# Kernel tuning notes

Hardware: AMD Instinct MI355X
Metric: run time of the kernel (lower is better)

Reference implementation:

```python
import jax, jax.numpy as jnp
import numpy as np

IMG_SIZE = 416
STRIDES = (8, 16, 32)
NUM_CLASSES = 43
RADIUS = 1
ALPHA, GAMMA = 0.25, 2.0
LAMBDA_CLS, LAMBDA_BOX, LAMBDA_OBJ = 0.5, 7.5, 1.0


def _bce_logits(x, t):
    # stable binary_cross_entropy_with_logits, elementwise
    return jnp.maximum(x, 0.0) - x * t + jnp.log1p(jnp.exp(-jnp.abs(x)))


def _focal(x, t):
    bce = _bce_logits(x, t)
    pt = jnp.exp(-bce)
    return ALPHA * (1.0 - pt) ** GAMMA * bce


def _decode_boxes(reg_flat, stride, H, W):
    # reg_flat: [B, H*W, 4] -> boxes [B, H*W, 4] in pixel x1y1x2y2
    gy, gx = jnp.meshgrid(jnp.arange(H), jnp.arange(W), indexing='ij')
    grid = jnp.stack([gx, gy], axis=-1).reshape(-1, 2).astype(reg_flat.dtype)  # [A,2]
    xy = (grid[None] + reg_flat[..., :2]) * stride
    wh = jnp.exp(jnp.clip(reg_flat[..., 2:], -10.0, 10.0)) * stride
    return jnp.concatenate([xy - wh * 0.5, xy + wh * 0.5], axis=-1)


def _iou(pb, tb):
    # elementwise IoU over last dim=4 boxes; pb, tb: [..., 4]
    ix1 = jnp.maximum(pb[..., 0], tb[..., 0])
    iy1 = jnp.maximum(pb[..., 1], tb[..., 1])
    ix2 = jnp.minimum(pb[..., 2], tb[..., 2])
    iy2 = jnp.minimum(pb[..., 3], tb[..., 3])
    inter = jnp.clip(ix2 - ix1, 0.0) * jnp.clip(iy2 - iy1, 0.0)
    pa = (pb[..., 2] - pb[..., 0]) * (pb[..., 3] - pb[..., 1])
    ta = (tb[..., 2] - tb[..., 0]) * (tb[..., 3] - tb[..., 1])
    return inter / (pa + ta - inter + 1e-7)


def _assign(bboxes_px, labels, stride, H, W, C):
    # Vectorized SimpleCenterAssigner. Sequential scan over max_obj preserves
    B, M = labels.shape
    A = H * W
    cx = (bboxes_px[..., 0] + bboxes_px[..., 2]) * 0.5  # [B,M]
    cy = (bboxes_px[..., 1] + bboxes_px[..., 3]) * 0.5
    gx = jnp.clip((cx / stride).astype(jnp.int32), 0, W - 1)
    gy = jnp.clip((cy / stride).astype(jnp.int32), 0, H - 1)
    valid = labels >= 0
    offs = jnp.arange(-RADIUS, RADIUS + 1)
    dys, dxs = jnp.meshgrid(offs, offs, indexing='ij')
    dys, dxs = dys.reshape(-1), dxs.reshape(-1)  # [K=9]
    K = dys.shape[0]
    b_idx = jnp.broadcast_to(jnp.arange(B)[:, None], (B, K))

    def step(carry, xs):
        tl, tb, ts, fg = carry
        gx_m, gy_m, lab_m, box_m, val_m = xs  # one gt per batch element
        ax = gx_m[:, None] + dxs[None, :]  # [B,K]
        ay = gy_m[:, None] + dys[None, :]
        inb = (ax >= 0) & (ax < W) & (ay >= 0) & (ay < H) & val_m[:, None]
        idx = jnp.where(inb, ay * W + ax, A)  # invalid writes routed to pad slot A
        lab_c = jnp.clip(lab_m, 0, C - 1)
        fg = fg.at[b_idx, idx].set(True)
        tl = tl.at[b_idx, idx].set(jnp.broadcast_to(lab_m[:, None], (B, K)))
        tb = tb.at[b_idx, idx].set(jnp.broadcast_to(box_m[:, None, :], (B, K, 4)))
        ts = ts.at[b_idx, idx, jnp.broadcast_to(lab_c[:, None], (B, K))].set(1.0)
        return (tl, tb, ts, fg), None

    init = (jnp.full((B, A + 1), -1, jnp.int32),
            jnp.zeros((B, A + 1, 4), bboxes_px.dtype),
            jnp.zeros((B, A + 1, C), bboxes_px.dtype),
            jnp.zeros((B, A + 1), bool))
    xs = (gx.T, gy.T, labels.T, jnp.transpose(bboxes_px, (1, 0, 2)), valid.T)
    (tl, tb, ts, fg), _ = jax.lax.scan(step, init, xs)
    return tl[:, :A], tb[:, :A], ts[:, :A], fg[:, :A]


def _scale_loss(cls, reg, obj, bboxes_px, labels, stride, C):
    B, _, H, W = cls.shape
    A = H * W
    cls_f = jnp.transpose(cls, (0, 2, 3, 1)).reshape(B, A, C)
    reg_f = jnp.transpose(reg, (0, 2, 3, 1)).reshape(B, A, 4)
    obj_f = jnp.transpose(obj, (0, 2, 3, 1)).reshape(B, A)
    boxes = _decode_boxes(reg_f, stride, H, W)
    _, tb, ts, fg = _assign(bboxes_px, labels, stride, H, W, C)
    fgf = fg.astype(cls_f.dtype)
    num_fg = jnp.maximum(fgf.sum(), 1.0)
    # focal loss mean over [num_fg, C] selected elements
    cls_loss = (_focal(cls_f, ts) * fgf[..., None]).sum() / (num_fg * C)
    # IoU loss mean over fg anchors
    box_loss = ((1.0 - _iou(boxes, tb)) * fgf).sum() / num_fg
    # obj BCE sum over all anchors / num_fg, target = fg mask
    obj_loss = _bce_logits(obj_f, fgf).sum() / num_fg
    return cls_loss, box_loss, obj_loss


def _v3_loss(cls0, reg0, obj0, cls1, reg1, obj1, cls2, reg2, obj2, bboxes, labels):
    bboxes_px = bboxes * IMG_SIZE
    preds = [(cls0, reg0, obj0), (cls1, reg1, obj1), (cls2, reg2, obj2)]
    tot_cls = tot_box = tot_obj = 0.0
    for (c, r, o), s in zip(preds, STRIDES):
        cl, bl, ol = _scale_loss(c, r, o, bboxes_px, labels, s, NUM_CLASSES)
        tot_cls = tot_cls + cl
        tot_box = tot_box + bl
        tot_obj = tot_obj + ol
    n = len(preds)
    return (LAMBDA_CLS * tot_cls + LAMBDA_BOX * tot_box + LAMBDA_OBJ * tot_obj) / n


def setup_inputs() -> dict:
    key = jax.random.key(0)
    ks = jax.random.split(key, 12)
    B, M = 128, 50
    shapes = [(52, 43), (52, 4), (52, 1), (26, 43), (26, 4), (26, 1), (13, 43), (13, 4), (13, 1)]
    names = ['cls0', 'reg0', 'obj0', 'cls1', 'reg1', 'obj1', 'cls2', 'reg2', 'obj2']
    inp = {}
    for i, (nm, (hw, c)) in enumerate(zip(names, shapes)):
        inp[nm] = jax.random.normal(ks[i], (B, c, hw, hw), dtype=jnp.float32)
    # normalized [0,1] x1y1x2y2 gt boxes with x1<x2, y1<y2
    u = jax.random.uniform(ks[9], (B, M, 4), dtype=jnp.float32)
    cx, cy = u[..., 0], u[..., 1]
    w = 0.02 + 0.2 * u[..., 2]
    h = 0.02 + 0.2 * u[..., 3]
    inp['bboxes'] = jnp.stack([jnp.clip(cx - w / 2, 0, 1), jnp.clip(cy - h / 2, 0, 1),
                               jnp.clip(cx + w / 2, 0, 1), jnp.clip(cy + h / 2, 0, 1)], axis=-1)
    inp['labels'] = jax.random.randint(ks[10], (B, M), 0, 43, dtype=jnp.int32)
    return inp


def reference(cls0, reg0, obj0, cls1, reg1, obj1, cls2, reg2, obj2, bboxes, labels):
    return _v3_loss(cls0, reg0, obj0, cls1, reg1, obj1, cls2, reg2, obj2, bboxes, labels)
```

## Files before the change

### kernel.cpp

```cpp
#include <hip/hip_runtime.h>
#include <math.h>

#define BB 128
#define MM 50
#define CC 43
#define IMGF 416.0f

#define NBLK0 1408
#define NBLK01 1792
#define NBLK_TOTAL 1920

__device__ __forceinline__ float focal_fast(float x, bool t) {
    float e = __expf(-fabsf(x));
    float denom = 1.0f + e;
    float l = __logf(denom);
    float bce = fmaxf(x, 0.0f) - (t ? x : 0.0f) + l;
    float r = __builtin_amdgcn_rcpf(denom);
    float sig = (x >= 0.0f) ? r : e * r;
    float pt = t ? sig : 1.0f - sig;
    float om = 1.0f - pt;
    return 0.25f * om * om * bce;
}

__device__ __forceinline__ float bce_fast(float x, bool t) {
    float e = __expf(-fabsf(x));
    float l = __logf(1.0f + e);
    return fmaxf(x, 0.0f) - (t ? x : 0.0f) + l;
}

__global__ __launch_bounds__(256) void v3_main(
    const float* __restrict__ cls0, const float* __restrict__ reg0, const float* __restrict__ obj0,
    const float* __restrict__ cls1, const float* __restrict__ reg1, const float* __restrict__ obj1,
    const float* __restrict__ cls2, const float* __restrict__ reg2, const float* __restrict__ obj2,
    const float* __restrict__ bboxes, const int* __restrict__ labels,
    float* __restrict__ partials)
{
    const int bid = blockIdx.x;
    int s, b, chunk;
    if (bid < NBLK0)       { s = 0; b = bid / 11; chunk = bid - 11 * b; }
    else if (bid < NBLK01) { int r = bid - NBLK0; s = 1; b = r / 3; chunk = r - 3 * b; }
    else                   { s = 2; b = bid - NBLK01; chunk = 0; }

    int W, A; float strd, inv_strd;
    const float *cls, *reg, *obj;
    if (s == 0)      { W = 52; A = 2704; strd = 8.f;  inv_strd = 0.125f;   cls = cls0; reg = reg0; obj = obj0; }
    else if (s == 1) { W = 26; A = 676;  strd = 16.f; inv_strd = 0.0625f;  cls = cls1; reg = reg1; obj = obj1; }
    else             { W = 13; A = 169;  strd = 32.f; inv_strd = 0.03125f; cls = cls2; reg = reg2; obj = obj2; }

    const int tid = threadIdx.x;
    const int lane = tid & 63, wid = tid >> 6;
    const int a_lo = chunk << 8;
    const int a_hi = min(a_lo + 255, A - 1);
    const int a = a_lo + tid;
    const bool active = (a < A);

    __shared__ int    s_lab[MM];
    __shared__ float4 s_boxv[MM];
    __shared__ unsigned s_glo[256], s_ghi[256];

    s_glo[tid] = 0u; s_ghi[tid] = 0u;
    int gx = -1, gy = -1, my_lab = -1;
    if (tid < MM) {
        my_lab = labels[b * MM + tid];
        float4 bb = ((const float4*)bboxes)[b * MM + tid];
        float4 pb = make_float4(bb.x * IMGF, bb.y * IMGF, bb.z * IMGF, bb.w * IMGF);
        s_boxv[tid] = pb;
        s_lab[tid] = min(max(my_lab, 0), CC - 1);
        float cx = (pb.x + pb.z) * 0.5f;
        float cy = (pb.y + pb.w) * 0.5f;
        gx = (int)(cx * inv_strd); gx = min(max(gx, 0), W - 1);
        gy = (int)(cy * inv_strd); gy = min(max(gy, 0), W - 1);
    }
    __syncthreads();

    if (tid < MM && my_lab >= 0) {
        unsigned bit = 1u << (tid & 31);
        bool is_hi = (tid >= 32);
        #pragma unroll
        for (int dy = -1; dy <= 1; ++dy) {
            int yy = gy + dy;
            if ((unsigned)yy < (unsigned)W) {
                #pragma unroll
                for (int dx = -1; dx <= 1; ++dx) {
                    int xx = gx + dx;
                    if ((unsigned)xx < (unsigned)W) {
                        int ac = yy * W + xx;
                        if (ac >= a_lo && ac <= a_hi) {
                            if (is_hi) atomicOr(&s_ghi[ac - a_lo], bit);
                            else       atomicOr(&s_glo[ac - a_lo], bit);
                        }
                    }
                }
            }
        }
    }
    __syncthreads();

    int ay;
    if (s == 0) ay = a / 52; else if (s == 1) ay = a / 26; else ay = a / 13;
    const int ax = a - ay * W;

    const unsigned glo = s_glo[tid], ghi = s_ghi[tid];
    const bool fg = (glo | ghi) != 0u;

    float obj_t = 0.f, cls_t = 0.f, box_t = 0.f, nfg = 0.f;
    if (active) {
        float xo = obj[(size_t)b * A + a];
        obj_t = bce_fast(xo, fg);
    }
    if (fg) {
        nfg = 1.0f;

        float xs[CC];
        const float* cp = cls + (size_t)b * CC * A + a;
        #pragma unroll
        for (int c = 0; c < CC; ++c) xs[c] = cp[(size_t)c * A];
        const float* rp = reg + (size_t)b * 4 * A + a;
        float rx = rp[0], ry = rp[(size_t)A], rw = rp[(size_t)2 * A], rh = rp[(size_t)3 * A];

        unsigned lo = 0u, hi = 0u;
        unsigned t = glo;
        while (t) {
            int m = __builtin_ctz(t); t &= t - 1;
            int lc = s_lab[m];
            if (lc < 32) lo |= 1u << lc; else hi |= 1u << (lc - 32);
        }
        t = ghi;
        while (t) {
            int m = 32 + __builtin_ctz(t); t &= t - 1;
            int lc = s_lab[m];
            if (lc < 32) lo |= 1u << lc; else hi |= 1u << (lc - 32);
        }
        int mstar = ghi ? (32 + 31 - __builtin_clz(ghi)) : (31 - __builtin_clz(glo));
        float4 tb = s_boxv[mstar];

        float px = ((float)ax + rx) * strd;
        float py = ((float)ay + ry) * strd;
        rw = fminf(fmaxf(rw, -10.0f), 10.0f);
        rh = fminf(fmaxf(rh, -10.0f), 10.0f);
        float pw = __expf(rw) * strd;
        float ph = __expf(rh) * strd;
        float p0 = px - pw * 0.5f, p1 = py - ph * 0.5f;
        float p2 = px + pw * 0.5f, p3 = py + ph * 0.5f;
        float ix1 = fmaxf(p0, tb.x), iy1 = fmaxf(p1, tb.y);
        float ix2 = fminf(p2, tb.z), iy2 = fminf(p3, tb.w);
        float inter = fmaxf(ix2 - ix1, 0.0f) * fmaxf(iy2 - iy1, 0.0f);
        float pa = (p2 - p0) * (p3 - p1);
        float ta = (tb.z - tb.x) * (tb.w - tb.y);
        float iou = inter / (pa + ta - inter + 1e-7f);
        box_t = 1.0f - iou;

        float acc = 0.0f;
        #pragma unroll
        for (int c = 0; c < CC; ++c) {
            bool bit = (c < 32) ? (((lo >> c) & 1u) != 0u) : (((hi >> (c - 32)) & 1u) != 0u);
            acc += focal_fast(xs[c], bit);
        }
        cls_t = acc;
    }

    for (int off = 32; off > 0; off >>= 1) {
        obj_t += __shfl_xor(obj_t, off);
        cls_t += __shfl_xor(cls_t, off);
        box_t += __shfl_xor(box_t, off);
        nfg   += __shfl_xor(nfg,   off);
    }
    __shared__ float s_red[4][4];
    if (lane == 0) {
        s_red[wid][0] = obj_t; s_red[wid][1] = cls_t;
        s_red[wid][2] = box_t; s_red[wid][3] = nfg;
    }
    __syncthreads();
    if (tid == 0) {
        float o = 0.f, c = 0.f, bx = 0.f, nf = 0.f;
        for (int w = 0; w < 4; ++w) {
            o += s_red[w][0]; c += s_red[w][1]; bx += s_red[w][2]; nf += s_red[w][3];
        }
        float* p = partials + (size_t)bid * 4;
        p[0] = o; p[1] = c; p[2] = bx; p[3] = nf;
    }
}

__global__ __launch_bounds__(256) void v3_final(const float* __restrict__ partials,
                                                float* __restrict__ out)
{
    const int tid = threadIdx.x;
    double o[3] = {0, 0, 0}, c[3] = {0, 0, 0}, bx[3] = {0, 0, 0}, nf[3] = {0, 0, 0};
    for (int i = tid; i < NBLK_TOTAL; i += 256) {
        int s = (i < NBLK0) ? 0 : ((i < NBLK01) ? 1 : 2);
        const float* p = partials + (size_t)i * 4;
        o[s]  += (double)p[0];
        c[s]  += (double)p[1];
        bx[s] += (double)p[2];
        nf[s] += (double)p[3];
    }
    for (int off = 32; off > 0; off >>= 1) {
        for (int s = 0; s < 3; ++s) {
            o[s]  += __shfl_xor(o[s],  off);
            c[s]  += __shfl_xor(c[s],  off);
            bx[s] += __shfl_xor(bx[s], off);
            nf[s] += __shfl_xor(nf[s], off);
        }
    }
    __shared__ double s_red[4][12];
    int wid = tid >> 6, lane = tid & 63;
    if (lane == 0) {
        for (int s = 0; s < 3; ++s) {
            s_red[wid][s * 4 + 0] = o[s];
            s_red[wid][s * 4 + 1] = c[s];
            s_red[wid][s * 4 + 2] = bx[s];
            s_red[wid][s * 4 + 3] = nf[s];
        }
    }
    __syncthreads();
    if (tid == 0) {
        double total = 0.0;
        for (int s = 0; s < 3; ++s) {
            double os = 0, cs = 0, bs = 0, ns = 0;
            for (int w = 0; w < 4; ++w) {
                os += s_red[w][s * 4 + 0];
                cs += s_red[w][s * 4 + 1];
                bs += s_red[w][s * 4 + 2];
                ns += s_red[w][s * 4 + 3];
            }
            double n = (ns > 1.0) ? ns : 1.0;
            total += 0.5 * (cs / (n * (double)CC)) + 7.5 * (bs / n) + 1.0 * (os / n);
        }
        out[0] = (float)(total / 3.0);
    }
}

extern "C" void kernel_launch(void* const* d_in, const int* in_sizes, int n_in,
                              void* d_out, int out_size, void* d_ws, size_t ws_size,
                              hipStream_t stream) {
    const float* cls0 = (const float*)d_in[0];
    const float* reg0 = (const float*)d_in[1];
    const float* obj0 = (const float*)d_in[2];
    const float* cls1 = (const float*)d_in[3];
    const float* reg1 = (const float*)d_in[4];
    const float* obj1 = (const float*)d_in[5];
    const float* cls2 = (const float*)d_in[6];
    const float* reg2 = (const float*)d_in[7];
    const float* obj2 = (const float*)d_in[8];
    const float* bboxes = (const float*)d_in[9];
    const int*   labels = (const int*)d_in[10];

    float* partials = (float*)d_ws;

    v3_main<<<NBLK_TOTAL, 256, 0, stream>>>(cls0, reg0, obj0, cls1, reg1, obj1,
                                            cls2, reg2, obj2, bboxes, labels,
                                            partials);
    v3_final<<<1, 256, 0, stream>>>(partials, (float*)d_out);
}
```

Measured before the change: 37.18 us.

## Redistribute class focal loss across waves with vectorized float4 anchor loads

The per-thread class-loss loop over 43 strided channels, run only by foreground threads, becomes a block-wide pass. Each wave handles a subset of channels and each lane loads four consecutive anchors with float4 loads. Per-anchor label bitmasks are shared through LDS so any lane can build targets. This removes warp divergence and widens memory transactions. In exchange it reads class logits for all anchors in the chunk, and adds an extra barrier and a separate scalar tail path.

```diff
diff --git a/kernel.cpp b/kernel.cpp
--- a/kernel.cpp
+++ b/kernel.cpp
@@ -56,7 +56,8 @@
 
     __shared__ int    s_lab[MM];
     __shared__ float4 s_boxv[MM];
-    __shared__ unsigned s_glo[256], s_ghi[256];
+    __shared__ alignas(16) unsigned s_glo[256];
+    __shared__ alignas(16) unsigned s_ghi[256];
 
     s_glo[tid] = 0u; s_ghi[tid] = 0u;
     int gx = -1, gy = -1, my_lab = -1;
@@ -103,22 +104,14 @@
     const unsigned glo = s_glo[tid], ghi = s_ghi[tid];
     const bool fg = (glo | ghi) != 0u;
 
-    float obj_t = 0.f, cls_t = 0.f, box_t = 0.f, nfg = 0.f;
+    float obj_t = 0.f, box_t = 0.f, nfg = 0.f;
     if (active) {
         float xo = obj[(size_t)b * A + a];
         obj_t = bce_fast(xo, fg);
     }
+    unsigned lo = 0u, hi = 0u;
     if (fg) {
         nfg = 1.0f;
-
-        float xs[CC];
-        const float* cp = cls + (size_t)b * CC * A + a;
-        #pragma unroll
-        for (int c = 0; c < CC; ++c) xs[c] = cp[(size_t)c * A];
-        const float* rp = reg + (size_t)b * 4 * A + a;
-        float rx = rp[0], ry = rp[(size_t)A], rw = rp[(size_t)2 * A], rh = rp[(size_t)3 * A];
-
-        unsigned lo = 0u, hi = 0u;
         unsigned t = glo;
         while (t) {
             int m = __builtin_ctz(t); t &= t - 1;
@@ -134,6 +127,8 @@
         int mstar = ghi ? (32 + 31 - __builtin_clz(ghi)) : (31 - __builtin_clz(glo));
         float4 tb = s_boxv[mstar];
 
+        const float* rp = reg + (size_t)b * 4 * A + a;
+        float rx = rp[0], ry = rp[(size_t)A], rw = rp[(size_t)2 * A], rh = rp[(size_t)3 * A];
         float px = ((float)ax + rx) * strd;
         float py = ((float)ay + ry) * strd;
         rw = fminf(fmaxf(rw, -10.0f), 10.0f);
@@ -149,14 +144,59 @@
         float ta = (tb.z - tb.x) * (tb.w - tb.y);
         float iou = inter / (pa + ta - inter + 1e-7f);
         box_t = 1.0f - iou;
-
-        float acc = 0.0f;
-        #pragma unroll
-        for (int c = 0; c < CC; ++c) {
-            bool bit = (c < 32) ? (((lo >> c) & 1u) != 0u) : (((hi >> (c - 32)) & 1u) != 0u);
-            acc += focal_fast(xs[c], bit);
-        }
-        cls_t = acc;
+    }
+
+    s_glo[tid] = lo;
+    s_ghi[tid] = hi;
+    __syncthreads();
+
+    float cls_t = 0.f;
+    {
+        const float* __restrict__ cbase = cls + (size_t)b * CC * A;
+        const bool tail = (a_hi - a_lo) < 255;
+        const int au = a_lo + 4 * lane;
+        const uint4 lo4 = *reinterpret_cast<const uint4*>(&s_glo[4 * lane]);
+        const uint4 hi4 = *reinterpret_cast<const uint4*>(&s_ghi[4 * lane]);
+        const bool f0 = (lo4.x | hi4.x) != 0u;
+        const bool f1 = (lo4.y | hi4.y) != 0u;
+        const bool f2 = (lo4.z | hi4.z) != 0u;
+        const bool f3 = (lo4.w | hi4.w) != 0u;
+        if (!tail) {
+            #pragma unroll
+            for (int cb = 0; cb < 11; ++cb) {
+                const int c = wid + 4 * cb;
+                if (c < CC) {
+                    const float4 x = *reinterpret_cast<const float4*>(cbase + (size_t)c * A + au);
+                    const bool b0 = ((c < 32) ? (lo4.x >> c) : (hi4.x >> (c - 32))) & 1u;
+                    const bool b1 = ((c < 32) ? (lo4.y >> c) : (hi4.y >> (c - 32))) & 1u;
+                    const bool b2 = ((c < 32) ? (lo4.z >> c) : (hi4.z >> (c - 32))) & 1u;
+                    const bool b3 = ((c < 32) ? (lo4.w >> c) : (hi4.w >> (c - 32))) & 1u;
+                    cls_t += f0 ? focal_fast(x.x, b0) : 0.f;
+                    cls_t += f1 ? focal_fast(x.y, b1) : 0.f;
+                    cls_t += f2 ? focal_fast(x.z, b2) : 0.f;
+                    cls_t += f3 ? focal_fast(x.w, b3) : 0.f;
+                }
+            }
+        } else {
+            const int i0 = min(au + 0, A - 1), i1 = min(au + 1, A - 1);
+            const int i2 = min(au + 2, A - 1), i3 = min(au + 3, A - 1);
+            #pragma unroll
+            for (int cb = 0; cb < 11; ++cb) {
+                const int c = wid + 4 * cb;
+                if (c < CC) {
+                    const float* ch = cbase + (size_t)c * A;
+                    const float x0 = ch[i0], x1 = ch[i1], x2 = ch[i2], x3 = ch[i3];
+                    const bool b0 = ((c < 32) ? (lo4.x >> c) : (hi4.x >> (c - 32))) & 1u;
+                    const bool b1 = ((c < 32) ? (lo4.y >> c) : (hi4.y >> (c - 32))) & 1u;
+                    const bool b2 = ((c < 32) ? (lo4.z >> c) : (hi4.z >> (c - 32))) & 1u;
+                    const bool b3 = ((c < 32) ? (lo4.w >> c) : (hi4.w >> (c - 32))) & 1u;
+                    cls_t += f0 ? focal_fast(x0, b0) : 0.f;
+                    cls_t += f1 ? focal_fast(x1, b1) : 0.f;
+                    cls_t += f2 ? focal_fast(x2, b2) : 0.f;
+                    cls_t += f3 ? focal_fast(x3, b3) : 0.f;
+                }
+            }
+        }
     }
 
     for (int off = 32; off > 0; off >>= 1) {
```

Measured after the change: 38.15 us. 1.03x slower.
